# Kernel optimization log

Hardware: AMD Instinct MI355X
Metric: run time of the kernel (lower is better)

The kernel has to match this reference:

```python
import jax, jax.numpy as jnp
import numpy as np

B, S, D, CH = 1024, 64, 256, 1024


def setup_inputs() -> dict:
    key = jax.random.key(0)
    ks = jax.random.split(key, 8)
    sc = 0.05
    return {
        "local_descs_t": jax.random.normal(ks[0], (B, S, D), jnp.float32),
        "local_descs_rot": jax.random.normal(ks[1], (B, S, D), jnp.float32),
        "W_scene": jax.random.normal(ks[2], (2 * D, 1), jnp.float32) * sc,
        "b_scene": jnp.zeros((1,), jnp.float32),
        "Wt_h": jax.random.normal(ks[3], (S, D, CH), jnp.float32) * sc,
        "bt_h": jnp.zeros((S, CH), jnp.float32),
        "Wt_o": jax.random.normal(ks[4], (S, CH, 3), jnp.float32) * sc,
        "bt_o": jnp.zeros((S, 3), jnp.float32),
        "Wr_h": jax.random.normal(ks[5], (S, D, CH), jnp.float32) * sc,
        "br_h": jnp.zeros((S, CH), jnp.float32),
        "Wr_o": jax.random.normal(ks[6], (S, CH, 4), jnp.float32) * sc,
        "br_o": jnp.zeros((S, 4), jnp.float32),
    }


def reference(local_descs_t, local_descs_rot, W_scene, b_scene,
              Wt_h, bt_h, Wt_o, bt_o, Wr_h, br_h, Wr_o, br_o):
    # scene classifier: Linear(2D -> 1) on concat descriptors, log-softmax over scenes
    cat = jnp.concatenate((local_descs_t, local_descs_rot), axis=2)  # [B,S,2D]
    logits = jnp.einsum('bsd,do->bso', cat, W_scene)[..., 0] + b_scene[0]  # [B,S]
    scene_log_distr = jax.nn.log_softmax(logits, axis=1)
    max_idx = jnp.argmax(scene_log_distr, axis=1)  # [B] top-1 scene per sample

    b = jnp.arange(local_descs_t.shape[0])
    g_t = local_descs_t[b, max_idx]      # [B,D] one-hot gather of selected scene
    g_rot = local_descs_rot[b, max_idx]  # [B,D]

    h_t = jax.nn.gelu(jnp.einsum('bd,bdh->bh', g_t, Wt_h[max_idx]) + bt_h[max_idx],
                      approximate=False)
    x_t = jnp.einsum('bh,bho->bo', h_t, Wt_o[max_idx]) + bt_o[max_idx]  # [B,3]
    h_r = jax.nn.gelu(jnp.einsum('bd,bdh->bh', g_rot, Wr_h[max_idx]) + br_h[max_idx],
                      approximate=False)
    x_rot = jnp.einsum('bh,bho->bo', h_r, Wr_o[max_idx]) + br_o[max_idx]  # [B,4]

    expected_pose = jnp.concatenate((x_t, x_rot), axis=1)  # [B,7]
    return expected_pose, scene_log_distr
```

## Files before the change

### kernel.cpp

```cpp
#include <hip/hip_runtime.h>
#include <math.h>

#define BN 1024
#define SN 64
#define DN 256
#define CHN 1024
#define GRP 16

__device__ __forceinline__ float gelu_exact(float x) {
    return 0.5f * x * (1.0f + erff(x * 0.70710678118654752440f));
}

__global__ __launch_bounds__(256) void k_scene(
    const float* __restrict__ dt, const float* __restrict__ dr,
    const float* __restrict__ Wsc, const float* __restrict__ bsc,
    float* __restrict__ out_logd, int* __restrict__ max_idx)
{
    int b = blockIdx.x;
    int tid = threadIdx.x;
    int lane = tid & 63;
    int wave = tid >> 6;
    __shared__ float part[SN][65];
    __shared__ float logits[SN];

    float4 wt = *(const float4*)&Wsc[4 * lane];
    float4 wr = *(const float4*)&Wsc[DN + 4 * lane];
    const float* pt = dt + (size_t)b * SN * DN + 4 * lane;
    const float* pr = dr + (size_t)b * SN * DN + 4 * lane;
    float bias0 = bsc[0];

    float p[16];
    #pragma unroll 4
    for (int k = 0; k < 16; k++) {
        int s = wave * 16 + k;
        float4 t4 = *(const float4*)&pt[s * DN];
        float4 r4 = *(const float4*)&pr[s * DN];
        p[k] = t4.x * wt.x + t4.y * wt.y + t4.z * wt.z + t4.w * wt.w
             + r4.x * wr.x + r4.y * wr.y + r4.z * wr.z + r4.w * wr.w;
    }
    #pragma unroll
    for (int k = 0; k < 16; k++) part[wave * 16 + k][lane] = p[k];
    __syncthreads();

    {
        int s = tid >> 2, q = tid & 3;
        float sum = 0.f;
        #pragma unroll
        for (int j = 0; j < 16; j++) sum += part[s][q * 16 + j];
        sum += __shfl_xor(sum, 1);
        sum += __shfl_xor(sum, 2);
        if (q == 0) logits[s] = sum + bias0;
    }
    __syncthreads();

    if (wave == 0) {
        float l = logits[lane];
        float m = l; int idx = lane;
        #pragma unroll
        for (int off = 32; off >= 1; off >>= 1) {
            float om = __shfl_xor(m, off);
            int oidx = __shfl_xor(idx, off);
            if (om > m || (om == m && oidx < idx)) { m = om; idx = oidx; }
        }
        float e = expf(l - m);
        float ssum = e;
        #pragma unroll
        for (int off = 32; off >= 1; off >>= 1) ssum += __shfl_xor(ssum, off);
        float logZ = m + logf(ssum);
        out_logd[b * SN + lane] = l - logZ;
        if (lane == 0) max_idx[b] = idx;
    }
}

__global__ __launch_bounds__(256) void k_init_pose(
    const int* __restrict__ max_idx,
    const float* __restrict__ bt_o, const float* __restrict__ br_o,
    float* __restrict__ pose)
{
    int t = blockIdx.x * blockDim.x + threadIdx.x;
    if (t >= BN * 7) return;
    int b = t / 7, o = t % 7;
    int s = max_idx[b];
    pose[t] = (o < 3) ? bt_o[s * 3 + o] : br_o[s * 4 + (o - 3)];
}

__global__ __launch_bounds__(256) void k_bin(
    const int* __restrict__ max_idx, int* __restrict__ counts, int* __restrict__ lists)
{
    int b = blockIdx.x * blockDim.x + threadIdx.x;
    if (b >= BN) return;
    int s = max_idx[b];
    int pos = atomicAdd(&counts[s], 1);
    lists[s * BN + pos] = b;
}

__global__ __launch_bounds__(256) void k_expert(
    const float* __restrict__ dt, const float* __restrict__ dr,
    const float* __restrict__ Wt_h, const float* __restrict__ bt_h, const float* __restrict__ Wt_o,
    const float* __restrict__ Wr_h, const float* __restrict__ br_h, const float* __restrict__ Wr_o,
    const int* __restrict__ counts, const int* __restrict__ lists,
    float* __restrict__ pose)
{
    int x = blockIdx.x;
    int s = x >> 2;
    int z = (x >> 1) & 1;
    int hh = x & 1;
    int grp = blockIdx.y;
    int cnt = counts[s];
    int base = grp * GRP;
    if (base >= cnt) return;
    int n = min(GRP, cnt - base);

    const float* Wh; const float* bh; const float* Wo; const float* descs; int no; int ob;
    if (z == 0) {
        Wh = Wt_h + (size_t)s * DN * CHN; bh = bt_h + s * CHN;
        Wo = Wt_o + (size_t)s * CHN * 3;  descs = dt; no = 3; ob = 0;
    } else {
        Wh = Wr_h + (size_t)s * DN * CHN; bh = br_h + s * CHN;
        Wo = Wr_o + (size_t)s * CHN * 4;  descs = dr; no = 4; ob = 3;
    }

    __shared__ float g[GRP][DN];
    __shared__ int bl[GRP];
    int tid = threadIdx.x;

    for (int i = 0; i < GRP; i++) {
        float v = 0.f;
        int bi = 0;
        if (i < n) {
            bi = lists[s * BN + base + i];
            v = descs[(size_t)bi * SN * DN + s * DN + tid];
        }
        g[i][tid] = v;
        if (tid == 0) bl[i] = bi;
    }
    __syncthreads();

    int h0 = hh * 512 + tid * 2;
    float2 acc[GRP];
    #pragma unroll
    for (int i = 0; i < GRP; i++) acc[i] = make_float2(0.f, 0.f);

    for (int d = 0; d < DN; d += 8) {
        float2 w[8];
        #pragma unroll
        for (int r = 0; r < 8; r++)
            w[r] = *(const float2*)&Wh[(size_t)(d + r) * CHN + h0];
        #pragma unroll
        for (int i = 0; i < GRP; i++) {
            float4 ga = *(const float4*)&g[i][d];
            float4 gb = *(const float4*)&g[i][d + 4];
            acc[i].x += ga.x * w[0].x + ga.y * w[1].x + ga.z * w[2].x + ga.w * w[3].x
                      + gb.x * w[4].x + gb.y * w[5].x + gb.z * w[6].x + gb.w * w[7].x;
            acc[i].y += ga.x * w[0].y + ga.y * w[1].y + ga.z * w[2].y + ga.w * w[3].y
                      + gb.x * w[4].y + gb.y * w[5].y + gb.z * w[6].y + gb.w * w[7].y;
        }
    }

    float b0 = bh[h0], b1 = bh[h0 + 1];
    int lane = tid & 63;
    for (int i = 0; i < n; i++) {
        float h0v = gelu_exact(acc[i].x + b0);
        float h1v = gelu_exact(acc[i].y + b1);
        for (int o = 0; o < no; o++) {
            float p = h0v * Wo[h0 * no + o] + h1v * Wo[(h0 + 1) * no + o];
            #pragma unroll
            for (int off = 32; off >= 1; off >>= 1) p += __shfl_down(p, off);
            if (lane == 0) atomicAdd(&pose[bl[i] * 7 + ob + o], p);
        }
    }
}

extern "C" void kernel_launch(void* const* d_in, const int* in_sizes, int n_in,
                              void* d_out, int out_size, void* d_ws, size_t ws_size,
                              hipStream_t stream) {
    const float* dt    = (const float*)d_in[0];
    const float* dr    = (const float*)d_in[1];
    const float* Wsc   = (const float*)d_in[2];
    const float* bsc   = (const float*)d_in[3];
    const float* Wt_h  = (const float*)d_in[4];
    const float* bt_h  = (const float*)d_in[5];
    const float* Wt_o  = (const float*)d_in[6];
    const float* bt_o  = (const float*)d_in[7];
    const float* Wr_h  = (const float*)d_in[8];
    const float* br_h  = (const float*)d_in[9];
    const float* Wr_o  = (const float*)d_in[10];
    const float* br_o  = (const float*)d_in[11];

    float* pose = (float*)d_out;
    float* logd = (float*)d_out + BN * 7;

    int* max_idx = (int*)d_ws;
    int* counts  = (int*)((char*)d_ws + 4096);
    int* lists   = (int*)((char*)d_ws + 8192);

    hipMemsetAsync(counts, 0, SN * sizeof(int), stream);

    k_scene<<<BN, 256, 0, stream>>>(dt, dr, Wsc, bsc, logd, max_idx);
    k_init_pose<<<(BN * 7 + 255) / 256, 256, 0, stream>>>(max_idx, bt_o, br_o, pose);
    k_bin<<<(BN + 255) / 256, 256, 0, stream>>>(max_idx, counts, lists);
    k_expert<<<dim3(256, 64), 256, 0, stream>>>(
        dt, dr, Wt_h, bt_h, Wt_o, Wr_h, br_h, Wr_o, counts, lists, pose);
}
```

Before: 332.8 us.

## Compact expert grid with prefix-sum scheduling, fuse init/bin kernels, double-buffer weights

Merges the pose-init and binning kernels into one launch. Replaces the sparse 256x64 expert grid, where most blocks exit early, with a dense 1D grid of 128-thread blocks. Each block finds its scene and group from a wave-level prefix sum over per-scene group counts. The weight loads are double-buffered so the next 8 rows arrive while the current ones are used, and the output weights are hoisted into registers. The cost is a serial scan per block to locate its scene, and a grid sized at 1024 that assumes enough groups exist.

```diff
diff --git a/kernel.cpp b/kernel.cpp
--- a/kernel.cpp
+++ b/kernel.cpp
@@ -30,7 +30,7 @@
     float bias0 = bsc[0];
 
     float p[16];
-    #pragma unroll 4
+    #pragma unroll 8
     for (int k = 0; k < 16; k++) {
         int s = wave * 16 + k;
         float4 t4 = *(const float4*)&pt[s * DN];
@@ -72,46 +72,66 @@
     }
 }
 
-__global__ __launch_bounds__(256) void k_init_pose(
+__global__ __launch_bounds__(256) void k_prep(
     const int* __restrict__ max_idx,
     const float* __restrict__ bt_o, const float* __restrict__ br_o,
-    float* __restrict__ pose)
+    float* __restrict__ pose, int* __restrict__ counts, int* __restrict__ lists)
 {
     int t = blockIdx.x * blockDim.x + threadIdx.x;
-    if (t >= BN * 7) return;
-    int b = t / 7, o = t % 7;
-    int s = max_idx[b];
-    pose[t] = (o < 3) ? bt_o[s * 3 + o] : br_o[s * 4 + (o - 3)];
-}
-
-__global__ __launch_bounds__(256) void k_bin(
-    const int* __restrict__ max_idx, int* __restrict__ counts, int* __restrict__ lists)
-{
-    int b = blockIdx.x * blockDim.x + threadIdx.x;
-    if (b >= BN) return;
-    int s = max_idx[b];
-    int pos = atomicAdd(&counts[s], 1);
-    lists[s * BN + pos] = b;
-}
-
-__global__ __launch_bounds__(256) void k_expert(
+    if (t < BN * 7) {
+        int b = t / 7, o = t % 7;
+        int s = max_idx[b];
+        pose[t] = (o < 3) ? bt_o[s * 3 + o] : br_o[s * 4 + (o - 3)];
+    }
+    if (t < BN) {
+        int s = max_idx[t];
+        int pos = atomicAdd(&counts[s], 1);
+        lists[s * BN + pos] = t;
+    }
+}
+
+__global__ __launch_bounds__(128) void k_expert(
     const float* __restrict__ dt, const float* __restrict__ dr,
     const float* __restrict__ Wt_h, const float* __restrict__ bt_h, const float* __restrict__ Wt_o,
     const float* __restrict__ Wr_h, const float* __restrict__ br_h, const float* __restrict__ Wr_o,
     const int* __restrict__ counts, const int* __restrict__ lists,
     float* __restrict__ pose)
 {
-    int x = blockIdx.x;
-    int s = x >> 2;
-    int z = (x >> 1) & 1;
-    int hh = x & 1;
-    int grp = blockIdx.y;
+    __shared__ float g[GRP][DN];
+    __shared__ int pref[SN + 1];
+    __shared__ int bl[GRP];
+    int tid = threadIdx.x;
+    int lane = tid & 63;
+    int wave = tid >> 6;
+
+    if (wave == 0) {
+        int c = counts[lane];
+        int ng = (c + 15) >> 4;
+        #pragma unroll
+        for (int off = 1; off < 64; off <<= 1) {
+            int v = __shfl_up(ng, off);
+            if (lane >= off) ng += v;
+        }
+        pref[lane + 1] = ng;
+        if (lane == 0) pref[0] = 0;
+    }
+    __syncthreads();
+
+    int q = blockIdx.x;
+    if (q >= pref[SN] * 8) return;
+
+    int s = 0;
+    while (pref[s + 1] * 8 <= q) s++;
+    int r = q - pref[s] * 8;
+    int grp = r >> 3;
+    int z = (r >> 2) & 1;
+    int c4 = r & 3;
+
     int cnt = counts[s];
     int base = grp * GRP;
-    if (base >= cnt) return;
     int n = min(GRP, cnt - base);
 
-    const float* Wh; const float* bh; const float* Wo; const float* descs; int no; int ob;
+    const float* Wh; const float* bh; const float* Wo; const float* descs; int no, ob;
     if (z == 0) {
         Wh = Wt_h + (size_t)s * DN * CHN; bh = bt_h + s * CHN;
         Wo = Wt_o + (size_t)s * CHN * 3;  descs = dt; no = 3; ob = 0;
@@ -120,53 +140,74 @@
         Wo = Wr_o + (size_t)s * CHN * 4;  descs = dr; no = 4; ob = 3;
     }
 
-    __shared__ float g[GRP][DN];
-    __shared__ int bl[GRP];
-    int tid = threadIdx.x;
-
     for (int i = 0; i < GRP; i++) {
-        float v = 0.f;
-        int bi = 0;
+        int bi = 0; float v0 = 0.f, v1 = 0.f;
         if (i < n) {
             bi = lists[s * BN + base + i];
-            v = descs[(size_t)bi * SN * DN + s * DN + tid];
-        }
-        g[i][tid] = v;
+            const float* src = descs + (size_t)bi * SN * DN + s * DN;
+            v0 = src[tid]; v1 = src[tid + 128];
+        }
+        g[i][tid] = v0; g[i][tid + 128] = v1;
         if (tid == 0) bl[i] = bi;
     }
     __syncthreads();
 
-    int h0 = hh * 512 + tid * 2;
+    int h0 = c4 * 256 + 2 * tid;
+    const float* wp = Wh + h0;
     float2 acc[GRP];
     #pragma unroll
     for (int i = 0; i < GRP; i++) acc[i] = make_float2(0.f, 0.f);
 
-    for (int d = 0; d < DN; d += 8) {
-        float2 w[8];
-        #pragma unroll
-        for (int r = 0; r < 8; r++)
-            w[r] = *(const float2*)&Wh[(size_t)(d + r) * CHN + h0];
+    float2 w0[8], w1[8];
+    #pragma unroll
+    for (int rr = 0; rr < 8; rr++) w0[rr] = *(const float2*)&wp[(size_t)rr * CHN];
+
+    for (int db = 0; db < DN; db += 16) {
+        #pragma unroll
+        for (int rr = 0; rr < 8; rr++) w1[rr] = *(const float2*)&wp[(size_t)(db + 8 + rr) * CHN];
         #pragma unroll
         for (int i = 0; i < GRP; i++) {
-            float4 ga = *(const float4*)&g[i][d];
-            float4 gb = *(const float4*)&g[i][d + 4];
-            acc[i].x += ga.x * w[0].x + ga.y * w[1].x + ga.z * w[2].x + ga.w * w[3].x
-                      + gb.x * w[4].x + gb.y * w[5].x + gb.z * w[6].x + gb.w * w[7].x;
-            acc[i].y += ga.x * w[0].y + ga.y * w[1].y + ga.z * w[2].y + ga.w * w[3].y
-                      + gb.x * w[4].y + gb.y * w[5].y + gb.z * w[6].y + gb.w * w[7].y;
-        }
-    }
-
-    float b0 = bh[h0], b1 = bh[h0 + 1];
-    int lane = tid & 63;
+            float4 ga = *(const float4*)&g[i][db];
+            float4 gb = *(const float4*)&g[i][db + 4];
+            acc[i].x += ga.x*w0[0].x + ga.y*w0[1].x + ga.z*w0[2].x + ga.w*w0[3].x
+                      + gb.x*w0[4].x + gb.y*w0[5].x + gb.z*w0[6].x + gb.w*w0[7].x;
+            acc[i].y += ga.x*w0[0].y + ga.y*w0[1].y + ga.z*w0[2].y + ga.w*w0[3].y
+                      + gb.x*w0[4].y + gb.y*w0[5].y + gb.z*w0[6].y + gb.w*w0[7].y;
+        }
+        if (db + 16 < DN) {
+            #pragma unroll
+            for (int rr = 0; rr < 8; rr++) w0[rr] = *(const float2*)&wp[(size_t)(db + 16 + rr) * CHN];
+        }
+        #pragma unroll
+        for (int i = 0; i < GRP; i++) {
+            float4 ga = *(const float4*)&g[i][db + 8];
+            float4 gb = *(const float4*)&g[i][db + 12];
+            acc[i].x += ga.x*w1[0].x + ga.y*w1[1].x + ga.z*w1[2].x + ga.w*w1[3].x
+                      + gb.x*w1[4].x + gb.y*w1[5].x + gb.z*w1[6].x + gb.w*w1[7].x;
+            acc[i].y += ga.x*w1[0].y + ga.y*w1[1].y + ga.z*w1[2].y + ga.w*w1[3].y
+                      + gb.x*w1[4].y + gb.y*w1[5].y + gb.z*w1[6].y + gb.w*w1[7].y;
+        }
+    }
+
+    float2 bv = *(const float2*)&bh[h0];
+    float wo0[4], wo1[4];
+    #pragma unroll
+    for (int o = 0; o < 4; o++) {
+        wo0[o] = (o < no) ? Wo[h0 * no + o] : 0.f;
+        wo1[o] = (o < no) ? Wo[(h0 + 1) * no + o] : 0.f;
+    }
+
     for (int i = 0; i < n; i++) {
-        float h0v = gelu_exact(acc[i].x + b0);
-        float h1v = gelu_exact(acc[i].y + b1);
-        for (int o = 0; o < no; o++) {
-            float p = h0v * Wo[h0 * no + o] + h1v * Wo[(h0 + 1) * no + o];
-            #pragma unroll
-            for (int off = 32; off >= 1; off >>= 1) p += __shfl_down(p, off);
-            if (lane == 0) atomicAdd(&pose[bl[i] * 7 + ob + o], p);
+        float h0v = gelu_exact(acc[i].x + bv.x);
+        float h1v = gelu_exact(acc[i].y + bv.y);
+        #pragma unroll
+        for (int o = 0; o < 4; o++) {
+            if (o < no) {
+                float p = h0v * wo0[o] + h1v * wo1[o];
+                #pragma unroll
+                for (int off = 32; off >= 1; off >>= 1) p += __shfl_down(p, off);
+                if (lane == 0) atomicAdd(&pose[bl[i] * 7 + ob + o], p);
+            }
         }
     }
 }
@@ -197,8 +238,7 @@
     hipMemsetAsync(counts, 0, SN * sizeof(int), stream);
 
     k_scene<<<BN, 256, 0, stream>>>(dt, dr, Wsc, bsc, logd, max_idx);
-    k_init_pose<<<(BN * 7 + 255) / 256, 256, 0, stream>>>(max_idx, bt_o, br_o, pose);
-    k_bin<<<(BN + 255) / 256, 256, 0, stream>>>(max_idx, counts, lists);
-    k_expert<<<dim3(256, 64), 256, 0, stream>>>(
+    k_prep<<<(BN * 7 + 255) / 256, 256, 0, stream>>>(max_idx, bt_o, br_o, pose, counts, lists);
+    k_expert<<<1024, 128, 0, stream>>>(
         dt, dr, Wt_h, bt_h, Wt_o, Wr_h, br_h, Wr_o, counts, lists, pose);
 }
```

Result: slower. 376.7 us (+13.2%).
